# Performance work log

Measured on AMD Instinct MI355X. Metric: run time of the kernel, lower is better.

## Reference

```python
import jax, jax.numpy as jnp
import numpy as np

N_NODES = 250000
N_EDGES = 4000000

def gcn_layer(x, src, dst, W, b, n_nodes):
    # PyG GCNConv: linear transform, add self-loops, symmetric normalization,
    # scatter-add aggregation at target nodes, then bias.
    xw = x @ W                                            # [N, out]
    deg = jax.ops.segment_sum(jnp.ones_like(src, dtype=xw.dtype), dst,
                              num_segments=n_nodes) + 1.0  # +1 for self loop
    dinv = deg ** -0.5                                     # deg >= 1 due to self loops
    norm = dinv[src] * dinv[dst]                           # [E]
    agg = jax.ops.segment_sum(norm[:, None] * xw[src], dst,
                              num_segments=n_nodes)        # neighbor messages
    out = agg + (dinv * dinv)[:, None] * xw + b            # self-loop message + bias
    return out


def setup_inputs() -> dict:
    key = jax.random.key(0)
    ks = jax.random.split(key, 8)
    x = jax.random.normal(ks[0], (N_NODES, 2), dtype=jnp.float32)
    edge_index = jax.random.randint(ks[1], (2, N_EDGES), 0, N_NODES, dtype=jnp.int64)
    def glorot(k, shape):
        lim = np.sqrt(6.0 / (shape[0] + shape[1]))
        return jax.random.uniform(k, shape, jnp.float32, -lim, lim)
    return {
        "x": x,
        "edge_index": edge_index,
        "W1": glorot(ks[2], (2, 16)),  "b1": jnp.zeros((16,), jnp.float32),
        "W2": glorot(ks[3], (16, 16)), "b2": jnp.zeros((16,), jnp.float32),
        "W3": glorot(ks[4], (16, 1)),  "b3": jnp.zeros((1,), jnp.float32),
    }


def reference(x, edge_index, W1, b1, W2, b2, W3, b3):
    src, dst = edge_index[0], edge_index[1]
    n = x.shape[0]
    h = jax.nn.relu(gcn_layer(x, src, dst, W1, b1, n))
    h = jax.nn.relu(gcn_layer(h, src, dst, W2, b2, n))
    return gcn_layer(h, src, dst, W3, b3, n)
```

## Files before the change

### kernel.cpp

```cpp
#include <hip/hip_runtime.h>


constexpr int K   = 977;
constexpr int NPW = 256;
constexpr int G   = 256;
constexpr int F   = 16;


__global__ __launch_bounds__(1024) void k_bcount(const int* __restrict__ dst,
        int* __restrict__ bcount, int E, int chunk) {
    __shared__ int h[K];
    for (int k = threadIdx.x; k < K; k += 1024) h[k] = 0;
    __syncthreads();
    int beg = blockIdx.x * chunk;
    int end = min(beg + chunk, E);
    for (int i = beg + threadIdx.x; i < end; i += 1024) {
        int d = __builtin_nontemporal_load(&dst[i]);
        atomicAdd(&h[d >> 8], 1);
    }
    __syncthreads();
    for (int k = threadIdx.x; k < K; k += 1024)
        bcount[blockIdx.x * K + k] = h[k];
}

__global__ __launch_bounds__(1024) void k_scan(int* __restrict__ bcount,
        int* __restrict__ colbase, int E) {
    __shared__ int tot[1024];
    int k = threadIdx.x;
    int s = 0;
    if (k < K) for (int b = 0; b < G; ++b) s += bcount[b * K + k];
    tot[k] = s;
    __syncthreads();
    for (int off = 1; off < 1024; off <<= 1) {
        int t = (k >= off) ? tot[k - off] : 0;
        __syncthreads();
        tot[k] += t;
        __syncthreads();
    }
    if (k < K) {
        int run = tot[k] - s;
        colbase[k] = run;
        for (int b = 0; b < G; ++b) {
            int t = bcount[b * K + k];
            bcount[b * K + k] = run;
            run += t;
        }
    }
    if (k == 0) colbase[K] = E;
}

__global__ __launch_bounds__(1024) void k_bfill(const int* __restrict__ src,
        const int* __restrict__ dst, const int* __restrict__ base,
        int* __restrict__ ent, int E, int chunk) {
    __shared__ int cur[K];
    for (int k = threadIdx.x; k < K; k += 1024)
        cur[k] = base[blockIdx.x * K + k];
    __syncthreads();
    int beg = blockIdx.x * chunk;
    int end = min(beg + chunk, E);
    for (int i = beg + threadIdx.x; i < end; i += 1024) {
        int d = __builtin_nontemporal_load(&dst[i]);
        int s = __builtin_nontemporal_load(&src[i]);
        int pos = atomicAdd(&cur[d >> 8], 1);
        ent[pos] = (s << 8) | (d & 255);
    }
}


__global__ __launch_bounds__(256) void k_prep(const int* __restrict__ ent,
        const int* __restrict__ colbase, const float* __restrict__ x,
        float* __restrict__ dinv, float* __restrict__ dx, int n) {
    __shared__ int h[NPW];
    h[threadIdx.x] = 0;
    __syncthreads();
    int beg = colbase[blockIdx.x], end = colbase[blockIdx.x + 1];
    for (int e = beg + threadIdx.x; e < end; e += 256) {
        int v = __builtin_nontemporal_load(&ent[e]);
        atomicAdd(&h[v & 255], 1);
    }
    __syncthreads();
    int i = (blockIdx.x << 8) + threadIdx.x;
    if (i < n) {
        float di = rsqrtf((float)h[threadIdx.x] + 1.0f);
        dinv[i] = di;
        float2 xv = reinterpret_cast<const float2*>(x)[i];
        reinterpret_cast<float2*>(dx)[i] = make_float2(di * xv.x, di * xv.y);
    }
}


__global__ __launch_bounds__(512) void k_layer1(const int* __restrict__ ent,
        const int* __restrict__ colbase, const float* __restrict__ dinv,
        const float* __restrict__ dx, const float* __restrict__ W1,
        const float* __restrict__ b1, float* __restrict__ dh1, int n) {
    __shared__ float acc[NPW * 2];
    __shared__ float sW[32];
    __shared__ float sb[16];
    if (threadIdx.x < 32) sW[threadIdx.x] = W1[threadIdx.x];
    if (threadIdx.x >= 32 && threadIdx.x < 48) sb[threadIdx.x - 32] = b1[threadIdx.x - 32];
    for (int t = threadIdx.x; t < NPW * 2; t += 512) acc[t] = 0.0f;
    __syncthreads();
    int beg = colbase[blockIdx.x], end = colbase[blockIdx.x + 1];
    for (int e = beg + threadIdx.x; e < end; e += 512) {
        int v = __builtin_nontemporal_load(&ent[e]);
        float2 xv = reinterpret_cast<const float2*>(dx)[v >> 8];
        int ld = v & 255;
        atomicAdd(&acc[ld * 2 + 0], xv.x);
        atomicAdd(&acc[ld * 2 + 1], xv.y);
    }
    __syncthreads();
    int r = threadIdx.x;
    if (r < NPW) {
        int i = (blockIdx.x << 8) + r;
        if (i < n) {
            float di = dinv[i];
            float2 ds = reinterpret_cast<const float2*>(dx)[i];
            float a0 = di * (acc[r * 2 + 0] + ds.x);
            float a1 = di * (acc[r * 2 + 1] + ds.y);
            float4* orow = reinterpret_cast<float4*>(dh1 + (size_t)i * F);
#pragma unroll
            for (int q = 0; q < 4; ++q) {
                float4 o;
                o.x = di * fmaxf(a0 * sW[4*q+0] + a1 * sW[16 + 4*q+0] + sb[4*q+0], 0.0f);
                o.y = di * fmaxf(a0 * sW[4*q+1] + a1 * sW[16 + 4*q+1] + sb[4*q+1], 0.0f);
                o.z = di * fmaxf(a0 * sW[4*q+2] + a1 * sW[16 + 4*q+2] + sb[4*q+2], 0.0f);
                o.w = di * fmaxf(a0 * sW[4*q+3] + a1 * sW[16 + 4*q+3] + sb[4*q+3], 0.0f);
                orow[q] = o;
            }
        }
    }
}


__global__ __launch_bounds__(512) void k_layer2(const int* __restrict__ ent,
        const int* __restrict__ colbase, const float* __restrict__ dinv,
        const float* __restrict__ dh1, const float* __restrict__ W2,
        const float* __restrict__ b2, const float* __restrict__ W3,
        float* __restrict__ dxw3, int n) {
    __shared__ float acc[NPW * 17];
    __shared__ float sW2[256];
    __shared__ float sW3[16];
    __shared__ float sb[16];
    if (threadIdx.x < 256) sW2[threadIdx.x] = W2[threadIdx.x];
    if (threadIdx.x >= 256 && threadIdx.x < 272) sW3[threadIdx.x - 256] = W3[threadIdx.x - 256];
    if (threadIdx.x >= 272 && threadIdx.x < 288) sb[threadIdx.x - 272] = b2[threadIdx.x - 272];
    for (int t = threadIdx.x; t < NPW * 17; t += 512) acc[t] = 0.0f;
    __syncthreads();
    int beg = colbase[blockIdx.x], end = colbase[blockIdx.x + 1];
    int g = threadIdx.x >> 4;
    int j = threadIdx.x & 15;
    for (int e = beg + g; e < end; e += 32) {
        int v = __builtin_nontemporal_load(&ent[e]);
        int s = v >> 8, ld = v & 255;
        atomicAdd(&acc[ld * 17 + j], dh1[(size_t)s * F + j]);
    }
    __syncthreads();
    int r = threadIdx.x;
    if (r < NPW) {
        int i = (blockIdx.x << 8) + r;
        if (i < n) {
            float di = dinv[i];
            const float* dh = dh1 + (size_t)i * F;
            float a[16];
#pragma unroll
            for (int q = 0; q < 16; ++q) a[q] = di * (acc[r * 17 + q] + dh[q]);
            float sum = 0.0f;
#pragma unroll
            for (int c = 0; c < 16; ++c) {
                float h = sb[c];
#pragma unroll
                for (int q = 0; q < 16; ++q) h += a[q] * sW2[q * 16 + c];
                sum += fmaxf(h, 0.0f) * sW3[c];
            }
            dxw3[i] = di * sum;
        }
    }
}


__global__ __launch_bounds__(512) void k_out(const int* __restrict__ ent,
        const int* __restrict__ colbase, const float* __restrict__ dinv,
        const float* __restrict__ dxw3, const float* __restrict__ b3,
        float* __restrict__ out, int n) {
    __shared__ float acc[NPW];
    for (int t = threadIdx.x; t < NPW; t += 512) acc[t] = 0.0f;
    __syncthreads();
    int beg = colbase[blockIdx.x], end = colbase[blockIdx.x + 1];
    for (int e = beg + threadIdx.x; e < end; e += 512) {
        int v = __builtin_nontemporal_load(&ent[e]);
        atomicAdd(&acc[v & 255], dxw3[v >> 8]);
    }
    __syncthreads();
    int r = threadIdx.x;
    if (r < NPW) {
        int i = (blockIdx.x << 8) + r;
        if (i < n) out[i] = dinv[i] * (acc[r] + dxw3[i]) + b3[0];
    }
}


extern "C" void kernel_launch(void* const* d_in, const int* in_sizes, int n_in,
                              void* d_out, int out_size, void* d_ws, size_t ws_size,
                              hipStream_t stream) {
    const float* x  = (const float*)d_in[0];
    const int*   ei = (const int*)d_in[1];
    const float* W1 = (const float*)d_in[2];
    const float* b1 = (const float*)d_in[3];
    const float* W2 = (const float*)d_in[4];
    const float* b2 = (const float*)d_in[5];
    const float* W3 = (const float*)d_in[6];
    const float* b3 = (const float*)d_in[7];

    const int n = in_sizes[0] / 2;
    const int E = in_sizes[1] / 2;
    const int* src = ei;
    const int* dst = ei + E;

    char* w = (char*)d_ws;
    int*   ent     = (int*)w;                    w += (size_t)E * 4;
    int*   bcount  = (int*)w;                    w += (size_t)G * K * 4;
    float* dinv    = (float*)w;                  w += (size_t)n * 4;
    float* dx      = (float*)w;                  w += (size_t)n * 2 * 4;
    float* dh1     = (float*)w;                  w += (size_t)n * F * 4;
    float* dxw3    = (float*)w;                  w += (size_t)n * 4;
    int*   colbase = (int*)w;                    w += (size_t)(K + 1) * 4;
    float* out     = (float*)d_out;

    const int chunk = (E + G - 1) / G;

    k_bcount<<<G, 1024, 0, stream>>>(dst, bcount, E, chunk);
    k_scan  <<<1, 1024, 0, stream>>>(bcount, colbase, E);
    k_bfill <<<G, 1024, 0, stream>>>(src, dst, bcount, ent, E, chunk);

    k_prep<<<K, 256, 0, stream>>>(ent, colbase, x, dinv, dx, n);

    k_layer1<<<K, 512, 0, stream>>>(ent, colbase, dinv, dx, W1, b1, dh1, n);
    k_layer2<<<K, 512, 0, stream>>>(ent, colbase, dinv, dh1, W2, b2, W3, dxw3, n);
    k_out   <<<K, 512, 0, stream>>>(ent, colbase, dinv, dxw3, b3, out, n);
}
```

Baseline: 552.9 us.

## Bucket edges by destination chunk and source group for gather locality

Edges are now bucketed into 2048-node destination chunks, each split into 8 source-range groups. Each gather pass therefore walks a bounded source window, which should improve L2 locality for dx, dh1 and dxw3 reads. Layer 2 is split into an aggregation kernel, with one block per (chunk, group) bucket that flushes its shared-memory accumulators to global memory with atomics, and a separate per-node transform kernel. The larger shared-memory accumulators (about 139KB in layer2a) and far fewer blocks in the other kernels (123 instead of 977) risk low occupancy, and the extra global atomics plus memset add traffic.

```diff
diff --git a/kernel.cpp b/kernel.cpp
--- a/kernel.cpp
+++ b/kernel.cpp
@@ -1,34 +1,35 @@
 #include <hip/hip_runtime.h>
 
 
-constexpr int K   = 977;
-constexpr int NPW = 256;
-constexpr int G   = 256;
-constexpr int F   = 16;
-
-
-__global__ __launch_bounds__(1024) void k_bcount(const int* __restrict__ dst,
-        int* __restrict__ bcount, int E, int chunk) {
-    __shared__ int h[K];
-    for (int k = threadIdx.x; k < K; k += 1024) h[k] = 0;
-    __syncthreads();
-    int beg = blockIdx.x * chunk;
-    int end = min(beg + chunk, E);
+constexpr int CH   = 2048;
+constexpr int G    = 256;
+constexpr int F    = 16;
+constexpr int BMAX = 1024;
+
+
+__global__ __launch_bounds__(1024) void k_bcount(const int* __restrict__ src,
+        const int* __restrict__ dst, int* __restrict__ bcount,
+        int E, int chunk, int npg, int B) {
+    __shared__ int h[BMAX];
+    for (int k = threadIdx.x; k < B; k += 1024) h[k] = 0;
+    __syncthreads();
+    int beg = blockIdx.x * chunk, end = min(beg + chunk, E);
     for (int i = beg + threadIdx.x; i < end; i += 1024) {
+        int s = __builtin_nontemporal_load(&src[i]);
         int d = __builtin_nontemporal_load(&dst[i]);
-        atomicAdd(&h[d >> 8], 1);
-    }
-    __syncthreads();
-    for (int k = threadIdx.x; k < K; k += 1024)
-        bcount[blockIdx.x * K + k] = h[k];
+        atomicAdd(&h[(d >> 11) * 8 + s / npg], 1);
+    }
+    __syncthreads();
+    for (int k = threadIdx.x; k < B; k += 1024)
+        bcount[blockIdx.x * B + k] = h[k];
 }
 
 __global__ __launch_bounds__(1024) void k_scan(int* __restrict__ bcount,
-        int* __restrict__ colbase, int E) {
+        int* __restrict__ colbase, int E, int B) {
     __shared__ int tot[1024];
     int k = threadIdx.x;
     int s = 0;
-    if (k < K) for (int b = 0; b < G; ++b) s += bcount[b * K + k];
+    if (k < B) for (int b = 0; b < G; ++b) s += bcount[b * B + k];
     tot[k] = s;
     __syncthreads();
     for (int off = 1; off < 1024; off <<= 1) {
@@ -37,54 +38,54 @@
         tot[k] += t;
         __syncthreads();
     }
-    if (k < K) {
+    if (k < B) {
         int run = tot[k] - s;
         colbase[k] = run;
         for (int b = 0; b < G; ++b) {
-            int t = bcount[b * K + k];
-            bcount[b * K + k] = run;
+            int t = bcount[b * B + k];
+            bcount[b * B + k] = run;
             run += t;
         }
     }
-    if (k == 0) colbase[K] = E;
+    if (k == 0) colbase[B] = E;
 }
 
 __global__ __launch_bounds__(1024) void k_bfill(const int* __restrict__ src,
         const int* __restrict__ dst, const int* __restrict__ base,
-        int* __restrict__ ent, int E, int chunk) {
-    __shared__ int cur[K];
-    for (int k = threadIdx.x; k < K; k += 1024)
-        cur[k] = base[blockIdx.x * K + k];
-    __syncthreads();
-    int beg = blockIdx.x * chunk;
-    int end = min(beg + chunk, E);
+        int* __restrict__ ent, int E, int chunk, int npg, int B) {
+    __shared__ int cur[BMAX];
+    for (int k = threadIdx.x; k < B; k += 1024)
+        cur[k] = base[blockIdx.x * B + k];
+    __syncthreads();
+    int beg = blockIdx.x * chunk, end = min(beg + chunk, E);
     for (int i = beg + threadIdx.x; i < end; i += 1024) {
+        int s = __builtin_nontemporal_load(&src[i]);
         int d = __builtin_nontemporal_load(&dst[i]);
-        int s = __builtin_nontemporal_load(&src[i]);
-        int pos = atomicAdd(&cur[d >> 8], 1);
-        ent[pos] = (s << 8) | (d & 255);
-    }
-}
-
-
-__global__ __launch_bounds__(256) void k_prep(const int* __restrict__ ent,
+        int g = s / npg;
+        int pos = atomicAdd(&cur[(d >> 11) * 8 + g], 1);
+        ent[pos] = ((s - g * npg) << 11) | (d & (CH - 1));
+    }
+}
+
+
+__global__ __launch_bounds__(512) void k_prep(const int* __restrict__ ent,
         const int* __restrict__ colbase, const float* __restrict__ x,
         float* __restrict__ dinv, float* __restrict__ dx, int n) {
-    __shared__ int h[NPW];
-    h[threadIdx.x] = 0;
-    __syncthreads();
-    int beg = colbase[blockIdx.x], end = colbase[blockIdx.x + 1];
-    for (int e = beg + threadIdx.x; e < end; e += 256) {
-        int v = __builtin_nontemporal_load(&ent[e]);
-        atomicAdd(&h[v & 255], 1);
-    }
-    __syncthreads();
-    int i = (blockIdx.x << 8) + threadIdx.x;
-    if (i < n) {
-        float di = rsqrtf((float)h[threadIdx.x] + 1.0f);
-        dinv[i] = di;
-        float2 xv = reinterpret_cast<const float2*>(x)[i];
-        reinterpret_cast<float2*>(dx)[i] = make_float2(di * xv.x, di * xv.y);
+    __shared__ int h[CH];
+    for (int t = threadIdx.x; t < CH; t += 512) h[t] = 0;
+    __syncthreads();
+    int beg = colbase[blockIdx.x * 8], end = colbase[blockIdx.x * 8 + 8];
+    for (int e = beg + threadIdx.x; e < end; e += 512)
+        atomicAdd(&h[ent[e] & (CH - 1)], 1);
+    __syncthreads();
+    for (int r = threadIdx.x; r < CH; r += 512) {
+        int i = blockIdx.x * CH + r;
+        if (i < n) {
+            float di = rsqrtf((float)h[r] + 1.0f);
+            dinv[i] = di;
+            float2 xv = reinterpret_cast<const float2*>(x)[i];
+            reinterpret_cast<float2*>(dx)[i] = make_float2(di * xv.x, di * xv.y);
+        }
     }
 }
 
@@ -92,26 +93,37 @@
 __global__ __launch_bounds__(512) void k_layer1(const int* __restrict__ ent,
         const int* __restrict__ colbase, const float* __restrict__ dinv,
         const float* __restrict__ dx, const float* __restrict__ W1,
-        const float* __restrict__ b1, float* __restrict__ dh1, int n) {
-    __shared__ float acc[NPW * 2];
+        const float* __restrict__ b1, float* __restrict__ dh1, int n, int npg) {
+    __shared__ float acc[CH * 2];
     __shared__ float sW[32];
     __shared__ float sb[16];
     if (threadIdx.x < 32) sW[threadIdx.x] = W1[threadIdx.x];
     if (threadIdx.x >= 32 && threadIdx.x < 48) sb[threadIdx.x - 32] = b1[threadIdx.x - 32];
-    for (int t = threadIdx.x; t < NPW * 2; t += 512) acc[t] = 0.0f;
-    __syncthreads();
-    int beg = colbase[blockIdx.x], end = colbase[blockIdx.x + 1];
-    for (int e = beg + threadIdx.x; e < end; e += 512) {
-        int v = __builtin_nontemporal_load(&ent[e]);
-        float2 xv = reinterpret_cast<const float2*>(dx)[v >> 8];
-        int ld = v & 255;
-        atomicAdd(&acc[ld * 2 + 0], xv.x);
-        atomicAdd(&acc[ld * 2 + 1], xv.y);
-    }
-    __syncthreads();
-    int r = threadIdx.x;
-    if (r < NPW) {
-        int i = (blockIdx.x << 8) + r;
+    for (int t = threadIdx.x; t < CH * 2; t += 512) acc[t] = 0.0f;
+    __syncthreads();
+    for (int g = 0; g < 8; ++g) {
+        int sbase = g * npg;
+        int beg = colbase[blockIdx.x * 8 + g], end = colbase[blockIdx.x * 8 + g + 1];
+        int e = beg + threadIdx.x;
+        for (; e + 512 < end; e += 1024) {
+            int v0 = ent[e], v1 = ent[e + 512];
+            float2 a0 = reinterpret_cast<const float2*>(dx)[sbase + (v0 >> 11)];
+            float2 a1 = reinterpret_cast<const float2*>(dx)[sbase + (v1 >> 11)];
+            atomicAdd(&acc[(v0 & (CH - 1)) * 2 + 0], a0.x);
+            atomicAdd(&acc[(v0 & (CH - 1)) * 2 + 1], a0.y);
+            atomicAdd(&acc[(v1 & (CH - 1)) * 2 + 0], a1.x);
+            atomicAdd(&acc[(v1 & (CH - 1)) * 2 + 1], a1.y);
+        }
+        if (e < end) {
+            int v = ent[e];
+            float2 a = reinterpret_cast<const float2*>(dx)[sbase + (v >> 11)];
+            atomicAdd(&acc[(v & (CH - 1)) * 2 + 0], a.x);
+            atomicAdd(&acc[(v & (CH - 1)) * 2 + 1], a.y);
+        }
+    }
+    __syncthreads();
+    for (int r = threadIdx.x; r < CH; r += 512) {
+        int i = blockIdx.x * CH + r;
         if (i < n) {
             float di = dinv[i];
             float2 ds = reinterpret_cast<const float2*>(dx)[i];
@@ -132,68 +144,102 @@
 }
 
 
-__global__ __launch_bounds__(512) void k_layer2(const int* __restrict__ ent,
-        const int* __restrict__ colbase, const float* __restrict__ dinv,
-        const float* __restrict__ dh1, const float* __restrict__ W2,
-        const float* __restrict__ b2, const float* __restrict__ W3,
-        float* __restrict__ dxw3, int n) {
-    __shared__ float acc[NPW * 17];
+__global__ __launch_bounds__(512) void k_layer2a(const int* __restrict__ ent,
+        const int* __restrict__ colbase, const float* __restrict__ dh1,
+        float* __restrict__ agg, int npg) {
+    __shared__ float acc[CH * 17];
+    for (int t = threadIdx.x; t < CH * 17; t += 512) acc[t] = 0.0f;
+    __syncthreads();
+    int g = blockIdx.x & 7;
+    int c = blockIdx.x >> 3;
+    int sbase = g * npg;
+    int beg = colbase[blockIdx.x], end = colbase[blockIdx.x + 1];
+    int q4 = (threadIdx.x & 3) * 4;
+    int e = beg + (threadIdx.x >> 2);
+    for (; e + 128 < end; e += 256) {
+        int v0 = ent[e], v1 = ent[e + 128];
+        float4 r0 = *reinterpret_cast<const float4*>(dh1 + (size_t)(sbase + (v0 >> 11)) * F + q4);
+        float4 r1 = *reinterpret_cast<const float4*>(dh1 + (size_t)(sbase + (v1 >> 11)) * F + q4);
+        int a0 = (v0 & (CH - 1)) * 17 + q4;
+        int a1 = (v1 & (CH - 1)) * 17 + q4;
+        atomicAdd(&acc[a0 + 0], r0.x); atomicAdd(&acc[a0 + 1], r0.y);
+        atomicAdd(&acc[a0 + 2], r0.z); atomicAdd(&acc[a0 + 3], r0.w);
+        atomicAdd(&acc[a1 + 0], r1.x); atomicAdd(&acc[a1 + 1], r1.y);
+        atomicAdd(&acc[a1 + 2], r1.z); atomicAdd(&acc[a1 + 3], r1.w);
+    }
+    for (; e < end; e += 128) {
+        int v = ent[e];
+        float4 r = *reinterpret_cast<const float4*>(dh1 + (size_t)(sbase + (v >> 11)) * F + q4);
+        int a0 = (v & (CH - 1)) * 17 + q4;
+        atomicAdd(&acc[a0 + 0], r.x); atomicAdd(&acc[a0 + 1], r.y);
+        atomicAdd(&acc[a0 + 2], r.z); atomicAdd(&acc[a0 + 3], r.w);
+    }
+    __syncthreads();
+    float* aggc = agg + (size_t)c * CH * F;
+    for (int t = threadIdx.x; t < CH * F; t += 512) {
+        int r = t >> 4, f = t & 15;
+        atomicAdd(&aggc[t], acc[r * 17 + f]);
+    }
+}
+
+
+__global__ __launch_bounds__(256) void k_layer2b(const float* __restrict__ agg,
+        const float* __restrict__ dh1, const float* __restrict__ dinv,
+        const float* __restrict__ W2, const float* __restrict__ b2,
+        const float* __restrict__ W3, float* __restrict__ dxw3, int n) {
     __shared__ float sW2[256];
     __shared__ float sW3[16];
     __shared__ float sb[16];
-    if (threadIdx.x < 256) sW2[threadIdx.x] = W2[threadIdx.x];
-    if (threadIdx.x >= 256 && threadIdx.x < 272) sW3[threadIdx.x - 256] = W3[threadIdx.x - 256];
-    if (threadIdx.x >= 272 && threadIdx.x < 288) sb[threadIdx.x - 272] = b2[threadIdx.x - 272];
-    for (int t = threadIdx.x; t < NPW * 17; t += 512) acc[t] = 0.0f;
-    __syncthreads();
-    int beg = colbase[blockIdx.x], end = colbase[blockIdx.x + 1];
-    int g = threadIdx.x >> 4;
-    int j = threadIdx.x & 15;
-    for (int e = beg + g; e < end; e += 32) {
-        int v = __builtin_nontemporal_load(&ent[e]);
-        int s = v >> 8, ld = v & 255;
-        atomicAdd(&acc[ld * 17 + j], dh1[(size_t)s * F + j]);
-    }
-    __syncthreads();
-    int r = threadIdx.x;
-    if (r < NPW) {
-        int i = (blockIdx.x << 8) + r;
-        if (i < n) {
-            float di = dinv[i];
-            const float* dh = dh1 + (size_t)i * F;
-            float a[16];
-#pragma unroll
-            for (int q = 0; q < 16; ++q) a[q] = di * (acc[r * 17 + q] + dh[q]);
-            float sum = 0.0f;
-#pragma unroll
-            for (int c = 0; c < 16; ++c) {
-                float h = sb[c];
-#pragma unroll
-                for (int q = 0; q < 16; ++q) h += a[q] * sW2[q * 16 + c];
-                sum += fmaxf(h, 0.0f) * sW3[c];
-            }
-            dxw3[i] = di * sum;
-        }
-    }
+    sW2[threadIdx.x] = W2[threadIdx.x];
+    if (threadIdx.x < 16) sW3[threadIdx.x] = W3[threadIdx.x];
+    else if (threadIdx.x < 32) sb[threadIdx.x - 16] = b2[threadIdx.x - 16];
+    __syncthreads();
+    int i = blockIdx.x * 256 + threadIdx.x;
+    if (i >= n) return;
+    float di = dinv[i];
+    const float* ag = agg + (size_t)i * F;
+    const float* dh = dh1 + (size_t)i * F;
+    float a[16];
+#pragma unroll
+    for (int q = 0; q < 16; ++q) a[q] = di * (ag[q] + dh[q]);
+    float sum = 0.0f;
+#pragma unroll
+    for (int c = 0; c < 16; ++c) {
+        float h = sb[c];
+#pragma unroll
+        for (int q = 0; q < 16; ++q) h += a[q] * sW2[q * 16 + c];
+        sum += fmaxf(h, 0.0f) * sW3[c];
+    }
+    dxw3[i] = di * sum;
 }
 
 
 __global__ __launch_bounds__(512) void k_out(const int* __restrict__ ent,
         const int* __restrict__ colbase, const float* __restrict__ dinv,
         const float* __restrict__ dxw3, const float* __restrict__ b3,
-        float* __restrict__ out, int n) {
-    __shared__ float acc[NPW];
-    for (int t = threadIdx.x; t < NPW; t += 512) acc[t] = 0.0f;
-    __syncthreads();
-    int beg = colbase[blockIdx.x], end = colbase[blockIdx.x + 1];
-    for (int e = beg + threadIdx.x; e < end; e += 512) {
-        int v = __builtin_nontemporal_load(&ent[e]);
-        atomicAdd(&acc[v & 255], dxw3[v >> 8]);
-    }
-    __syncthreads();
-    int r = threadIdx.x;
-    if (r < NPW) {
-        int i = (blockIdx.x << 8) + r;
+        float* __restrict__ out, int n, int npg) {
+    __shared__ float acc[CH];
+    for (int t = threadIdx.x; t < CH; t += 512) acc[t] = 0.0f;
+    __syncthreads();
+    for (int g = 0; g < 8; ++g) {
+        int sbase = g * npg;
+        int beg = colbase[blockIdx.x * 8 + g], end = colbase[blockIdx.x * 8 + g + 1];
+        int e = beg + threadIdx.x;
+        for (; e + 512 < end; e += 1024) {
+            int v0 = ent[e], v1 = ent[e + 512];
+            float s0 = dxw3[sbase + (v0 >> 11)];
+            float s1 = dxw3[sbase + (v1 >> 11)];
+            atomicAdd(&acc[v0 & (CH - 1)], s0);
+            atomicAdd(&acc[v1 & (CH - 1)], s1);
+        }
+        if (e < end) {
+            int v = ent[e];
+            atomicAdd(&acc[v & (CH - 1)], dxw3[sbase + (v >> 11)]);
+        }
+    }
+    __syncthreads();
+    for (int r = threadIdx.x; r < CH; r += 512) {
+        int i = blockIdx.x * CH + r;
         if (i < n) out[i] = dinv[i] * (acc[r] + dxw3[i]) + b3[0];
     }
 }
@@ -216,25 +262,35 @@
     const int* src = ei;
     const int* dst = ei + E;
 
+    const int NC  = (n + CH - 1) / CH;
+    const int B   = NC * 8;
+    const int npg = (n + 7) / 8;
+
     char* w = (char*)d_ws;
-    int*   ent     = (int*)w;                    w += (size_t)E * 4;
-    int*   bcount  = (int*)w;                    w += (size_t)G * K * 4;
-    float* dinv    = (float*)w;                  w += (size_t)n * 4;
-    float* dx      = (float*)w;                  w += (size_t)n * 2 * 4;
-    float* dh1     = (float*)w;                  w += (size_t)n * F * 4;
-    float* dxw3    = (float*)w;                  w += (size_t)n * 4;
-    int*   colbase = (int*)w;                    w += (size_t)(K + 1) * 4;
+    int*   ent     = (int*)w;                 w += (size_t)E * 4;
+    int*   bcount  = (int*)w;                 w += (size_t)G * B * 4;
+    int*   colbase = (int*)w;                 w += (size_t)(B + 1) * 4;
+    w = (char*)(((uintptr_t)w + 15) & ~(uintptr_t)15);
+    float* dinv    = (float*)w;               w += (size_t)n * 4;
+    float* dx      = (float*)w;               w += (size_t)n * 2 * 4;
+    float* dh1     = (float*)w;               w += (size_t)n * F * 4;
+    float* agg     = (float*)w;               w += (size_t)NC * CH * F * 4;
+    float* dxw3    = (float*)w;               w += (size_t)n * 4;
     float* out     = (float*)d_out;
 
     const int chunk = (E + G - 1) / G;
 
-    k_bcount<<<G, 1024, 0, stream>>>(dst, bcount, E, chunk);
-    k_scan  <<<1, 1024, 0, stream>>>(bcount, colbase, E);
-    k_bfill <<<G, 1024, 0, stream>>>(src, dst, bcount, ent, E, chunk);
-
-    k_prep<<<K, 256, 0, stream>>>(ent, colbase, x, dinv, dx, n);
-
-    k_layer1<<<K, 512, 0, stream>>>(ent, colbase, dinv, dx, W1, b1, dh1, n);
-    k_layer2<<<K, 512, 0, stream>>>(ent, colbase, dinv, dh1, W2, b2, W3, dxw3, n);
-    k_out   <<<K, 512, 0, stream>>>(ent, colbase, dinv, dxw3, b3, out, n);
-}
+    k_bcount<<<G, 1024, 0, stream>>>(src, dst, bcount, E, chunk, npg, B);
+    k_scan  <<<1, 1024, 0, stream>>>(bcount, colbase, E, B);
+    k_bfill <<<G, 1024, 0, stream>>>(src, dst, bcount, ent, E, chunk, npg, B);
+
+    k_prep<<<NC, 512, 0, stream>>>(ent, colbase, x, dinv, dx, n);
+
+    k_layer1<<<NC, 512, 0, stream>>>(ent, colbase, dinv, dx, W1, b1, dh1, n, npg);
+
+    hipMemsetAsync(agg, 0, (size_t)NC * CH * F * 4, stream);
+    k_layer2a<<<B, 512, 0, stream>>>(ent, colbase, dh1, agg, npg);
+    k_layer2b<<<(n + 255) / 256, 256, 0, stream>>>(agg, dh1, dinv, W2, b2, W3, dxw3, n);
+
+    k_out<<<NC, 512, 0, stream>>>(ent, colbase, dinv, dxw3, b3, out, n, npg);
+}
```

New measurement: 722.4 us. 1.31x slower.

## Split per-bucket aggregation into multi-block global-atomic scatter plus node-wise transform

Applied to the files above, without the earlier changes.

Each layer's fused kernel, which accumulated a 256-node bucket in shared memory, becomes two kernels. First, a scatter kernel splits each bucket across 8 or 16 blocks and adds into a zeroed global buffer with global atomics. Then a per-node kernel applies normalization, the weights, ReLU and bias. The goal is more parallelism per bucket and less load imbalance and low occupancy from one block per bucket. The cost is global atomic traffic, extra memsets and more launches.

```diff
diff --git a/kernel.cpp b/kernel.cpp
--- a/kernel.cpp
+++ b/kernel.cpp
@@ -12,8 +12,7 @@
     __shared__ int h[K];
     for (int k = threadIdx.x; k < K; k += 1024) h[k] = 0;
     __syncthreads();
-    int beg = blockIdx.x * chunk;
-    int end = min(beg + chunk, E);
+    int beg = blockIdx.x * chunk, end = min(beg + chunk, E);
     for (int i = beg + threadIdx.x; i < end; i += 1024) {
         int d = __builtin_nontemporal_load(&dst[i]);
         atomicAdd(&h[d >> 8], 1);
@@ -56,8 +55,7 @@
     for (int k = threadIdx.x; k < K; k += 1024)
         cur[k] = base[blockIdx.x * K + k];
     __syncthreads();
-    int beg = blockIdx.x * chunk;
-    int end = min(beg + chunk, E);
+    int beg = blockIdx.x * chunk, end = min(beg + chunk, E);
     for (int i = beg + threadIdx.x; i < end; i += 1024) {
         int d = __builtin_nontemporal_load(&dst[i]);
         int s = __builtin_nontemporal_load(&src[i]);
@@ -74,10 +72,8 @@
     h[threadIdx.x] = 0;
     __syncthreads();
     int beg = colbase[blockIdx.x], end = colbase[blockIdx.x + 1];
-    for (int e = beg + threadIdx.x; e < end; e += 256) {
-        int v = __builtin_nontemporal_load(&ent[e]);
-        atomicAdd(&h[v & 255], 1);
-    }
+    for (int e = beg + threadIdx.x; e < end; e += 256)
+        atomicAdd(&h[ent[e] & 255], 1);
     __syncthreads();
     int i = (blockIdx.x << 8) + threadIdx.x;
     if (i < n) {
@@ -89,113 +85,110 @@
 }
 
 
-__global__ __launch_bounds__(512) void k_layer1(const int* __restrict__ ent,
-        const int* __restrict__ colbase, const float* __restrict__ dinv,
-        const float* __restrict__ dx, const float* __restrict__ W1,
-        const float* __restrict__ b1, float* __restrict__ dh1, int n) {
-    __shared__ float acc[NPW * 2];
+__global__ __launch_bounds__(256) void k_scat2(const int* __restrict__ ent,
+        const int* __restrict__ colbase, const float* __restrict__ dx,
+        float* __restrict__ agg2) {
+    int k = blockIdx.x >> 3, seg = blockIdx.x & 7;
+    int beg = colbase[k], end = colbase[k + 1];
+    for (int e = beg + seg * 256 + threadIdx.x; e < end; e += 8 * 256) {
+        int v = ent[e];
+        float2 a = reinterpret_cast<const float2*>(dx)[v >> 8];
+        int d = (k << 8) + (v & 255);
+        atomicAdd(&agg2[d * 2 + 0], a.x);
+        atomicAdd(&agg2[d * 2 + 1], a.y);
+    }
+}
+
+__global__ __launch_bounds__(256) void k_l1b(const float* __restrict__ agg2,
+        const float* __restrict__ dx, const float* __restrict__ dinv,
+        const float* __restrict__ W1, const float* __restrict__ b1,
+        float* __restrict__ dh1, int n) {
     __shared__ float sW[32];
     __shared__ float sb[16];
     if (threadIdx.x < 32) sW[threadIdx.x] = W1[threadIdx.x];
     if (threadIdx.x >= 32 && threadIdx.x < 48) sb[threadIdx.x - 32] = b1[threadIdx.x - 32];
-    for (int t = threadIdx.x; t < NPW * 2; t += 512) acc[t] = 0.0f;
-    __syncthreads();
-    int beg = colbase[blockIdx.x], end = colbase[blockIdx.x + 1];
-    for (int e = beg + threadIdx.x; e < end; e += 512) {
-        int v = __builtin_nontemporal_load(&ent[e]);
-        float2 xv = reinterpret_cast<const float2*>(dx)[v >> 8];
-        int ld = v & 255;
-        atomicAdd(&acc[ld * 2 + 0], xv.x);
-        atomicAdd(&acc[ld * 2 + 1], xv.y);
-    }
-    __syncthreads();
-    int r = threadIdx.x;
-    if (r < NPW) {
-        int i = (blockIdx.x << 8) + r;
-        if (i < n) {
-            float di = dinv[i];
-            float2 ds = reinterpret_cast<const float2*>(dx)[i];
-            float a0 = di * (acc[r * 2 + 0] + ds.x);
-            float a1 = di * (acc[r * 2 + 1] + ds.y);
-            float4* orow = reinterpret_cast<float4*>(dh1 + (size_t)i * F);
-#pragma unroll
-            for (int q = 0; q < 4; ++q) {
-                float4 o;
-                o.x = di * fmaxf(a0 * sW[4*q+0] + a1 * sW[16 + 4*q+0] + sb[4*q+0], 0.0f);
-                o.y = di * fmaxf(a0 * sW[4*q+1] + a1 * sW[16 + 4*q+1] + sb[4*q+1], 0.0f);
-                o.z = di * fmaxf(a0 * sW[4*q+2] + a1 * sW[16 + 4*q+2] + sb[4*q+2], 0.0f);
-                o.w = di * fmaxf(a0 * sW[4*q+3] + a1 * sW[16 + 4*q+3] + sb[4*q+3], 0.0f);
-                orow[q] = o;
-            }
-        }
-    }
-}
-
-
-__global__ __launch_bounds__(512) void k_layer2(const int* __restrict__ ent,
-        const int* __restrict__ colbase, const float* __restrict__ dinv,
-        const float* __restrict__ dh1, const float* __restrict__ W2,
-        const float* __restrict__ b2, const float* __restrict__ W3,
-        float* __restrict__ dxw3, int n) {
-    __shared__ float acc[NPW * 17];
+    __syncthreads();
+    int i = blockIdx.x * 256 + threadIdx.x;
+    if (i >= n) return;
+    float di = dinv[i];
+    float2 ds = reinterpret_cast<const float2*>(dx)[i];
+    float2 ag = reinterpret_cast<const float2*>(agg2)[i];
+    float a0 = di * (ag.x + ds.x);
+    float a1 = di * (ag.y + ds.y);
+    float4* orow = reinterpret_cast<float4*>(dh1 + (size_t)i * F);
+#pragma unroll
+    for (int q = 0; q < 4; ++q) {
+        float4 o;
+        o.x = di * fmaxf(a0 * sW[4*q+0] + a1 * sW[16 + 4*q+0] + sb[4*q+0], 0.0f);
+        o.y = di * fmaxf(a0 * sW[4*q+1] + a1 * sW[16 + 4*q+1] + sb[4*q+1], 0.0f);
+        o.z = di * fmaxf(a0 * sW[4*q+2] + a1 * sW[16 + 4*q+2] + sb[4*q+2], 0.0f);
+        o.w = di * fmaxf(a0 * sW[4*q+3] + a1 * sW[16 + 4*q+3] + sb[4*q+3], 0.0f);
+        orow[q] = o;
+    }
+}
+
+
+__global__ __launch_bounds__(256) void k_scat16(const int* __restrict__ ent,
+        const int* __restrict__ colbase, const float* __restrict__ dh1,
+        float* __restrict__ agg16) {
+    int k = blockIdx.x >> 4, seg = blockIdx.x & 15;
+    int beg = colbase[k], end = colbase[k + 1];
+    int j = threadIdx.x & 15;
+    for (int e = beg + seg * 16 + (threadIdx.x >> 4); e < end; e += 16 * 16) {
+        int v = ent[e];
+        float val = dh1[(size_t)(v >> 8) * F + j];
+        atomicAdd(&agg16[((size_t)(k << 8) + (v & 255)) * F + j], val);
+    }
+}
+
+__global__ __launch_bounds__(256) void k_l2b(const float* __restrict__ agg16,
+        const float* __restrict__ dh1, const float* __restrict__ dinv,
+        const float* __restrict__ W2, const float* __restrict__ b2,
+        const float* __restrict__ W3, float* __restrict__ dxw3, int n) {
     __shared__ float sW2[256];
     __shared__ float sW3[16];
     __shared__ float sb[16];
-    if (threadIdx.x < 256) sW2[threadIdx.x] = W2[threadIdx.x];
-    if (threadIdx.x >= 256 && threadIdx.x < 272) sW3[threadIdx.x - 256] = W3[threadIdx.x - 256];
-    if (threadIdx.x >= 272 && threadIdx.x < 288) sb[threadIdx.x - 272] = b2[threadIdx.x - 272];
-    for (int t = threadIdx.x; t < NPW * 17; t += 512) acc[t] = 0.0f;
-    __syncthreads();
-    int beg = colbase[blockIdx.x], end = colbase[blockIdx.x + 1];
-    int g = threadIdx.x >> 4;
-    int j = threadIdx.x & 15;
-    for (int e = beg + g; e < end; e += 32) {
-        int v = __builtin_nontemporal_load(&ent[e]);
-        int s = v >> 8, ld = v & 255;
-        atomicAdd(&acc[ld * 17 + j], dh1[(size_t)s * F + j]);
-    }
-    __syncthreads();
-    int r = threadIdx.x;
-    if (r < NPW) {
-        int i = (blockIdx.x << 8) + r;
-        if (i < n) {
-            float di = dinv[i];
-            const float* dh = dh1 + (size_t)i * F;
-            float a[16];
-#pragma unroll
-            for (int q = 0; q < 16; ++q) a[q] = di * (acc[r * 17 + q] + dh[q]);
-            float sum = 0.0f;
-#pragma unroll
-            for (int c = 0; c < 16; ++c) {
-                float h = sb[c];
-#pragma unroll
-                for (int q = 0; q < 16; ++q) h += a[q] * sW2[q * 16 + c];
-                sum += fmaxf(h, 0.0f) * sW3[c];
-            }
-            dxw3[i] = di * sum;
-        }
-    }
-}
-
-
-__global__ __launch_bounds__(512) void k_out(const int* __restrict__ ent,
-        const int* __restrict__ colbase, const float* __restrict__ dinv,
-        const float* __restrict__ dxw3, const float* __restrict__ b3,
-        float* __restrict__ out, int n) {
-    __shared__ float acc[NPW];
-    for (int t = threadIdx.x; t < NPW; t += 512) acc[t] = 0.0f;
-    __syncthreads();
-    int beg = colbase[blockIdx.x], end = colbase[blockIdx.x + 1];
-    for (int e = beg + threadIdx.x; e < end; e += 512) {
-        int v = __builtin_nontemporal_load(&ent[e]);
-        atomicAdd(&acc[v & 255], dxw3[v >> 8]);
-    }
-    __syncthreads();
-    int r = threadIdx.x;
-    if (r < NPW) {
-        int i = (blockIdx.x << 8) + r;
-        if (i < n) out[i] = dinv[i] * (acc[r] + dxw3[i]) + b3[0];
-    }
+    sW2[threadIdx.x] = W2[threadIdx.x];
+    if (threadIdx.x < 16) sW3[threadIdx.x] = W3[threadIdx.x];
+    else if (threadIdx.x < 32) sb[threadIdx.x - 16] = b2[threadIdx.x - 16];
+    __syncthreads();
+    int i = blockIdx.x * 256 + threadIdx.x;
+    if (i >= n) return;
+    float di = dinv[i];
+    const float* ag = agg16 + (size_t)i * F;
+    const float* dh = dh1 + (size_t)i * F;
+    float a[16];
+#pragma unroll
+    for (int q = 0; q < 16; ++q) a[q] = di * (ag[q] + dh[q]);
+    float sum = 0.0f;
+#pragma unroll
+    for (int c = 0; c < 16; ++c) {
+        float h = sb[c];
+#pragma unroll
+        for (int q = 0; q < 16; ++q) h += a[q] * sW2[q * 16 + c];
+        sum += fmaxf(h, 0.0f) * sW3[c];
+    }
+    dxw3[i] = di * sum;
+}
+
+
+__global__ __launch_bounds__(256) void k_scat1(const int* __restrict__ ent,
+        const int* __restrict__ colbase, const float* __restrict__ dxw3,
+        float* __restrict__ agg1) {
+    int k = blockIdx.x >> 3, seg = blockIdx.x & 7;
+    int beg = colbase[k], end = colbase[k + 1];
+    for (int e = beg + seg * 256 + threadIdx.x; e < end; e += 8 * 256) {
+        int v = ent[e];
+        float s = dxw3[v >> 8];
+        atomicAdd(&agg1[(k << 8) + (v & 255)], s);
+    }
+}
+
+__global__ __launch_bounds__(256) void k_outb(const float* __restrict__ agg1,
+        const float* __restrict__ dxw3, const float* __restrict__ dinv,
+        const float* __restrict__ b3, float* __restrict__ out, int n) {
+    int i = blockIdx.x * 256 + threadIdx.x;
+    if (i < n) out[i] = dinv[i] * (agg1[i] + dxw3[i]) + b3[0];
 }
 
 
@@ -217,16 +210,22 @@
     const int* dst = ei + E;
 
     char* w = (char*)d_ws;
-    int*   ent     = (int*)w;                    w += (size_t)E * 4;
-    int*   bcount  = (int*)w;                    w += (size_t)G * K * 4;
-    float* dinv    = (float*)w;                  w += (size_t)n * 4;
-    float* dx      = (float*)w;                  w += (size_t)n * 2 * 4;
-    float* dh1     = (float*)w;                  w += (size_t)n * F * 4;
-    float* dxw3    = (float*)w;                  w += (size_t)n * 4;
-    int*   colbase = (int*)w;                    w += (size_t)(K + 1) * 4;
-    float* out     = (float*)d_out;
+    int*   ent     = (int*)w;                 w += (size_t)E * 4;
+    int*   bcount  = (int*)w;                 w += (size_t)G * K * 4;
+    int*   colbase = (int*)w;                 w += (size_t)(K + 1) * 4;
+    w = (char*)(((uintptr_t)w + 15) & ~(uintptr_t)15);
+    float* dinv    = (float*)w;               w += (size_t)n * 4;
+    float* dx      = (float*)w;               w += (size_t)n * 2 * 4;
+    float* dh1     = (float*)w;               w += (size_t)n * F * 4;
+    float* aggp    = (float*)w;               w += (size_t)n * F * 4;
+    float* dxw3    = (float*)w;               w += (size_t)n * 4;
+    float* agg2  = aggp;
+    float* agg16 = aggp;
+    float* agg1  = aggp;
+    float* out   = (float*)d_out;
 
     const int chunk = (E + G - 1) / G;
+    const int gridN = (n + 255) / 256;
 
     k_bcount<<<G, 1024, 0, stream>>>(dst, bcount, E, chunk);
     k_scan  <<<1, 1024, 0, stream>>>(bcount, colbase, E);
@@ -234,7 +233,15 @@
 
     k_prep<<<K, 256, 0, stream>>>(ent, colbase, x, dinv, dx, n);
 
-    k_layer1<<<K, 512, 0, stream>>>(ent, colbase, dinv, dx, W1, b1, dh1, n);
-    k_layer2<<<K, 512, 0, stream>>>(ent, colbase, dinv, dh1, W2, b2, W3, dxw3, n);
-    k_out   <<<K, 512, 0, stream>>>(ent, colbase, dinv, dxw3, b3, out, n);
-}
+    hipMemsetAsync(agg2, 0, (size_t)n * 2 * 4, stream);
+    k_scat2<<<K * 8, 256, 0, stream>>>(ent, colbase, dx, agg2);
+    k_l1b<<<gridN, 256, 0, stream>>>(agg2, dx, dinv, W1, b1, dh1, n);
+
+    hipMemsetAsync(agg16, 0, (size_t)n * F * 4, stream);
+    k_scat16<<<K * 16, 256, 0, stream>>>(ent, colbase, dh1, agg16);
+    k_l2b<<<gridN, 256, 0, stream>>>(agg16, dh1, dinv, W2, b2, W3, dxw3, n);
+
+    hipMemsetAsync(agg1, 0, (size_t)n * 4, stream);
+    k_scat1<<<K * 8, 256, 0, stream>>>(ent, colbase, dxw3, agg1);
+    k_outb<<<gridN, 256, 0, stream>>>(agg1, dxw3, dinv, b3, out, n);
+}
```

After: 869.0 us. 57.2% more time.
